# Optimization experiments

Measured on AMD Instinct MI355X. Metric: run time of the kernel, lower is better.

Reference implementation:

```python
import jax, jax.numpy as jnp
import numpy as np

DIM = 768
NUM_HEADS = 12
HEAD_DIM = DIM // NUM_HEADS
SCALE = HEAD_DIM ** -0.5
NEG = -9e15


def setup_inputs() -> dict:
    key = jax.random.key(0)
    ks = jax.random.split(key, 8)
    B, N, M, C = 4, 1024, 2048, DIM
    q = jax.random.normal(ks[0], (B, N, C), dtype=jnp.float32)
    kv = jax.random.normal(ks[1], (B, M, C), dtype=jnp.float32)
    mask = jax.random.randint(ks[2], (B, 1, N, M), 0, 2, dtype=jnp.int32)
    s = 1.0 / np.sqrt(C)
    Wq = jax.random.normal(ks[3], (C, C), dtype=jnp.float32) * s      # nn.Linear(dim, dim), no bias
    Wkv = jax.random.normal(ks[4], (2 * C, C), dtype=jnp.float32) * s  # nn.Linear(dim, 2*dim), no bias
    Wproj = jax.random.normal(ks[5], (C, C), dtype=jnp.float32) * s
    bproj = jax.random.normal(ks[6], (C,), dtype=jnp.float32) * s
    return {"q": q, "kv": kv, "Wq": Wq, "Wkv": Wkv, "Wproj": Wproj, "bproj": bproj, "mask": mask}


def reference(q, kv, Wq, Wkv, Wproj, bproj, mask):
    B, M, C = kv.shape
    _, N, _ = q.shape
    H, d = NUM_HEADS, HEAD_DIM
    # kv projection -> [B, M, 2, H, d] -> k, v: [B, H, M, d]
    kvp = (kv @ Wkv.T).reshape(B, M, 2, H, d)
    k = kvp[:, :, 0].transpose(0, 2, 1, 3)
    v = kvp[:, :, 1].transpose(0, 2, 1, 3)
    # q projection -> [B, H, N, d], pre-scaled
    qp = (q @ Wq.T).reshape(B, N, H, d).transpose(0, 2, 1, 3) * SCALE
    attn = jnp.einsum('bhnd,bhmd->bhnm', qp, k)  # [B, H, N, M]
    attn = jnp.where(mask == 0, NEG, attn)
    attn = jax.nn.softmax(attn, axis=-1)
    # attn_drop / proj_drop have rate 0.0 (eval): identity
    x = jnp.einsum('bhnm,bhmd->bhnd', attn, v)
    x = x.transpose(0, 2, 1, 3).reshape(B, N, C)
    x = x @ Wproj.T + bproj
    return x
```

## Files before the change

### kernel.cpp

```cpp
#include <hip/hip_runtime.h>
#include <hip/hip_bf16.h>


typedef short    s16x8  __attribute__((ext_vector_type(8)));
typedef short    s16x4  __attribute__((ext_vector_type(4)));
typedef float    f32x4  __attribute__((ext_vector_type(4)));
typedef _Float16 f16x8  __attribute__((ext_vector_type(8)));
typedef _Float16 f16x4  __attribute__((ext_vector_type(4)));
typedef _Float16 f16x2  __attribute__((ext_vector_type(2)));

#define NUM_H 12
#define DIM   768
#define NQ    1024
#define MK    2048
#define QK_SCALE_LOG2E 0.18033688f

__device__ __forceinline__ short f2h(float v) {
    _Float16 h = (_Float16)v;
    return __builtin_bit_cast(short, h);
}
__device__ __forceinline__ f32x4 mfma16x32(f16x8 a, f16x8 b, f32x4 c) {
    return __builtin_amdgcn_mfma_f32_16x16x32_f16(a, b, c, 0, 0, 0);
}
__device__ __forceinline__ f16x2 pk2h(float a, float b) {
    return __builtin_bit_cast(f16x2, __builtin_amdgcn_cvt_pkrtz(a, b));
}
__device__ __forceinline__ void gl_lds16(const short* g, short* l) {
    __builtin_amdgcn_global_load_lds(
        (const __attribute__((address_space(1))) unsigned int*)g,
        (__attribute__((address_space(3))) unsigned int*)l, 16, 0, 0);
}

__global__ __launch_bounds__(256) void prep_kernel(
    const float* __restrict__ q, const float* __restrict__ kv,
    const float* __restrict__ Wq, const float* __restrict__ Wkv,
    const float* __restrict__ Wp,
    short* __restrict__ q_h, short* __restrict__ kv_h,
    short* __restrict__ Wq_h, short* __restrict__ Wkv_h,
    short* __restrict__ Wp_h)
{
    int bid = blockIdx.x;
    const float* s; short* d; long base;
    if (bid < 1536)      { s = q;   d = q_h;   base = (long)bid * 2048; }
    else if (bid < 4608) { s = kv;  d = kv_h;  base = (long)(bid - 1536) * 2048; }
    else if (bid < 4896) { s = Wq;  d = Wq_h;  base = (long)(bid - 4608) * 2048; }
    else if (bid < 5472) { s = Wkv; d = Wkv_h; base = (long)(bid - 4896) * 2048; }
    else                 { s = Wp;  d = Wp_h;  base = (long)(bid - 5472) * 2048; }
    long i = base + threadIdx.x * 8;
    float4 a = *(const float4*)(s + i);
    float4 b = *(const float4*)(s + i + 4);
    s16x8 r;
    r[0] = f2h(a.x); r[1] = f2h(a.y); r[2] = f2h(a.z); r[3] = f2h(a.w);
    r[4] = f2h(b.x); r[5] = f2h(b.y); r[6] = f2h(b.z); r[7] = f2h(b.w);
    *(s16x8*)(d + i) = r;
}

__device__ __forceinline__ void gemm_core(
    short* smem,
    const short* __restrict__ A, const short* __restrict__ Bt,
    int mtiles, int mode, const float* __restrict__ bias,
    short* __restrict__ outb, short* __restrict__ outb2,
    float* __restrict__ outf, int bid)
{
    short (*As)[64] = (short(*)[64])smem;
    short (*Bs)[64] = (short(*)[64])(smem + 8192);

    int m0 = (bid % mtiles) << 7;
    int n0 = (bid / mtiles) << 7;
    int t = threadIdx.x;
    int w = t >> 6, lane = t & 63, quad = lane >> 4, l16 = lane & 15;
    int wm = (w & 1) << 6, wn = (w >> 1) << 6;

    f32x4 zero4 = {0.f, 0.f, 0.f, 0.f};
    f32x4 acc[4][4];
    for (int i = 0; i < 4; i++)
        for (int j = 0; j < 4; j++) acc[i][j] = zero4;

    const short* Ag = A + (long)(m0 + (w << 5) + (lane >> 3)) * DIM + ((lane & 7) << 3);
    const short* Bg = Bt + (long)(n0 + (w << 5) + (lane >> 3)) * DIM + ((lane & 7) << 3);
    short* Al = &As[w << 5][0];
    short* Bl = &Bs[w << 5][0];

    for (int kt = 0; kt < DIM; kt += 64) {
        __syncthreads();
        #pragma unroll
        for (int i = 0; i < 4; i++) {
            gl_lds16(Ag + (long)i * 8 * DIM + kt, Al + i * 512);
            gl_lds16(Bg + (long)i * 8 * DIM + kt, Bl + i * 512);
        }
        __syncthreads();
        #pragma unroll
        for (int kh = 0; kh < 2; kh++) {
            f16x8 af[4], bfr[4];
            #pragma unroll
            for (int i = 0; i < 4; i++)
                af[i] = __builtin_bit_cast(f16x8,
                    *(const s16x8*)&As[wm + i * 16 + l16][kh * 32 + quad * 8]);
            #pragma unroll
            for (int j = 0; j < 4; j++)
                bfr[j] = __builtin_bit_cast(f16x8,
                    *(const s16x8*)&Bs[wn + j * 16 + l16][kh * 32 + quad * 8]);
            #pragma unroll
            for (int i = 0; i < 4; i++)
                #pragma unroll
                for (int j = 0; j < 4; j++)
                    acc[i][j] = mfma16x32(af[i], bfr[j], acc[i][j]);
        }
    }

    __syncthreads();

    if (mode == 2) {
        #pragma unroll
        for (int i = 0; i < 4; i++)
            #pragma unroll
            for (int j = 0; j < 4; j++)
                #pragma unroll
                for (int r = 0; r < 4; r++) {
                    int row = m0 + wm + i * 16 + quad * 4 + r;
                    int col = n0 + wn + j * 16 + l16;
                    outf[(long)row * DIM + col] = acc[i][j][r] + bias[col];
                }
        return;
    }

    short (*Cs)[136] = (short(*)[136])smem;
    bool vreg = (mode == 1) && (n0 >= DIM);

    if (!vreg) {
        float sc = (mode == 0) ? QK_SCALE_LOG2E : 1.0f;
        #pragma unroll
        for (int i = 0; i < 4; i++)
            #pragma unroll
            for (int j = 0; j < 4; j++)
                #pragma unroll
                for (int r = 0; r < 4; r++)
                    Cs[wm + i * 16 + quad * 4 + r][wn + j * 16 + l16] =
                        f2h(acc[i][j][r] * sc);
    } else {
        #pragma unroll
        for (int i = 0; i < 4; i++)
            #pragma unroll
            for (int j = 0; j < 4; j++) {
                int c = wn + j * 16 + l16;
                int r0 = wm + i * 16 + quad * 4;
                s16x4 pk;
                pk[0] = f2h(acc[i][j][0]); pk[1] = f2h(acc[i][j][1]);
                pk[2] = f2h(acc[i][j][2]); pk[3] = f2h(acc[i][j][3]);
                *(s16x4*)&Cs[c][r0] = pk;
            }
    }
    __syncthreads();

    if (!vreg) {
        int hb2 = n0 >> 6;
        long rowsN = (mode == 0) ? NQ : MK;
        int b = (int)(m0 / rowsN);
        int rb = (int)(m0 % rowsN);
        short* ob0 = outb + ((long)(b * NUM_H + hb2) * rowsN + rb) * 64;
        short* ob1 = outb + ((long)(b * NUM_H + hb2 + 1) * rowsN + rb) * 64;
        #pragma unroll
        for (int k2 = 0; k2 < 8; k2++) {
            int ch = k2 * 256 + t;
            int half = ch >> 10, off = ch & 1023;
            s16x8 vd = *(const s16x8*)&Cs[off >> 3][(half << 6) + ((off & 7) << 3)];
            *(s16x8*)((half ? ob1 : ob0) + off * 8) = vd;
        }
    } else {
        int hb2 = (n0 - DIM) >> 6;
        int b = m0 >> 11, rb = m0 & 2047;
        #pragma unroll
        for (int k2 = 0; k2 < 8; k2++) {
            int ch = k2 * 256 + t;
            int c = ch >> 4, woff = (ch & 15) << 3;
            s16x8 vd = *(const s16x8*)&Cs[c][woff];
            int half = c >> 6, dd = c & 63;
            *(s16x8*)(outb2 + (((long)(b * NUM_H + hb2 + half) * 64 + dd) * MK + rb) + woff) = vd;
        }
    }
}

__global__ __launch_bounds__(256) void gemm12_kernel(
    const short* __restrict__ qh, const short* __restrict__ Wqh,
    const short* __restrict__ kvh, const short* __restrict__ Wkvh,
    short* __restrict__ qp, short* __restrict__ kk, short* __restrict__ vt,
    const int* __restrict__ mask, unsigned char* __restrict__ mbytes)
{
    __shared__ short smem[18432];
    int bid = blockIdx.x;
    if (bid >= 960) {
        long base = (long)(bid - 960) * 2048 + threadIdx.x * 8;
        int4 m0 = *(const int4*)(mask + base);
        int4 m1 = *(const int4*)(mask + base + 4);
        unsigned v = (unsigned)(m0.x != 0)        | ((unsigned)(m0.y != 0) << 1)
                   | ((unsigned)(m0.z != 0) << 2) | ((unsigned)(m0.w != 0) << 3)
                   | ((unsigned)(m1.x != 0) << 4) | ((unsigned)(m1.y != 0) << 5)
                   | ((unsigned)(m1.z != 0) << 6) | ((unsigned)(m1.w != 0) << 7);
        mbytes[base >> 3] = (unsigned char)v;
        return;
    }
    if (bid < 192)
        gemm_core(smem, qh, Wqh, 32, 0, nullptr, qp, nullptr, nullptr, bid);
    else
        gemm_core(smem, kvh, Wkvh, 64, 1, nullptr, kk, vt, nullptr, bid - 192);
}

__global__ __launch_bounds__(256) void gemm3_kernel(
    const short* __restrict__ xb, const short* __restrict__ Wph,
    const float* __restrict__ bias, float* __restrict__ out)
{
    __shared__ short smem[18432];
    gemm_core(smem, xb, Wph, 32, 2, bias, nullptr, nullptr, out, blockIdx.x);
}

__global__ __launch_bounds__(256) void attn_kernel(
    const short* __restrict__ qp, const short* __restrict__ kk,
    const short* __restrict__ vt, const unsigned* __restrict__ mb,
    short* __restrict__ xb)
{
    __shared__ short qs[64][72];
    __shared__ short ks[64][72];
    __shared__ short vs[64][72];

    int bid = blockIdx.x;
    int bh = bid % 48;
    int nt = bid / 48;
    int h = bh % NUM_H, b = bh / NUM_H;
    int n0 = nt << 6;
    int t = threadIdx.x, w = t >> 6, lane = t & 63, quad = lane >> 4, l16 = lane & 15;

    const short* qbase = qp + ((long)bh * NQ + n0) * 64;
    const short* kbase = kk + (long)bh * MK * 64;
    const short* vbase = vt + (long)bh * 64 * MK;
    const unsigned* mrow = mb + ((long)b * NQ + n0 + (w << 4) + l16) * 64;

    {
        int qr = t >> 2, c0 = (t & 3) << 4;
        *(s16x8*)&qs[qr][c0]     = *(const s16x8*)(qbase + qr * 64 + c0);
        *(s16x8*)&qs[qr][c0 + 8] = *(const s16x8*)(qbase + qr * 64 + c0 + 8);
    }
    __syncthreads();
    f16x8 bq[2];
    #pragma unroll
    for (int kh = 0; kh < 2; kh++)
        bq[kh] = __builtin_bit_cast(f16x8,
            *(const s16x8*)&qs[(w << 4) + l16][kh * 32 + quad * 8]);

    int sr = t >> 2, c0 = (t & 3) << 4;
    int pr = (sr & 32) + ((sr & 4) << 2) + ((sr & 24) >> 1) + (sr & 3);
    const short* kp = kbase + (long)sr * 64 + c0;
    const short* vp = vbase + (long)sr * MK + c0;

    s16x8 k0 = *(const s16x8*)(kp);
    s16x8 k1 = *(const s16x8*)(kp + 8);
    s16x8 v0 = *(const s16x8*)(vp);
    s16x8 v1 = *(const s16x8*)(vp + 8);
    uint2 mwv = *(const uint2*)(mrow);

    f32x4 zero4 = {0.f, 0.f, 0.f, 0.f};
    f32x4 o[4], ol = zero4;
    for (int j = 0; j < 4; j++) o[j] = zero4;
    const f16x8 ones = {(_Float16)1.f, (_Float16)1.f, (_Float16)1.f, (_Float16)1.f,
                        (_Float16)1.f, (_Float16)1.f, (_Float16)1.f, (_Float16)1.f};

    for (int mt = 0; mt < MK; mt += 64) {
        __syncthreads();
        *(s16x8*)&ks[pr][c0]     = k0;
        *(s16x8*)&ks[pr][c0 + 8] = k1;
        *(s16x8*)&vs[sr][c0]     = v0;
        *(s16x8*)&vs[sr][c0 + 8] = v1;
        unsigned cm0 = mwv.x, cm1 = mwv.y;
        __syncthreads();
        if (mt + 64 < MK) {
            k0 = *(const s16x8*)(kp + (long)(mt + 64) * 64);
            k1 = *(const s16x8*)(kp + (long)(mt + 64) * 64 + 8);
            v0 = *(const s16x8*)(vp + mt + 64);
            v1 = *(const s16x8*)(vp + mt + 64 + 8);
            mwv = *(const uint2*)(mrow + ((mt + 64) >> 5));
        }

        f32x4 s[4];
        #pragma unroll
        for (int jj = 0; jj < 4; jj++) s[jj] = zero4;
        #pragma unroll
        for (int kh = 0; kh < 2; kh++)
            #pragma unroll
            for (int jj = 0; jj < 4; jj++) {
                f16x8 ak = __builtin_bit_cast(f16x8,
                    *(const s16x8*)&ks[jj * 16 + l16][kh * 32 + quad * 8]);
                s[jj] = mfma16x32(ak, bq[kh], s[jj]);
            }

        f16x8 pa[2];
        #pragma unroll
        for (int j2 = 0; j2 < 2; j2++) {
            unsigned wsel = j2 ? cm1 : cm0;
            f16x2 pk[4];
            #pragma unroll
            for (int sub = 0; sub < 2; sub++) {
                unsigned bits = wsel >> ((quad << 3) + (sub << 2));
                const f32x4& sv = s[j2 * 2 + sub];
                float p0 = (bits & 1u)        ? __builtin_amdgcn_exp2f(sv[0]) : 0.f;
                float p1 = ((bits >> 1) & 1u) ? __builtin_amdgcn_exp2f(sv[1]) : 0.f;
                float p2 = ((bits >> 2) & 1u) ? __builtin_amdgcn_exp2f(sv[2]) : 0.f;
                float p3 = ((bits >> 3) & 1u) ? __builtin_amdgcn_exp2f(sv[3]) : 0.f;
                pk[sub * 2]     = pk2h(p0, p1);
                pk[sub * 2 + 1] = pk2h(p2, p3);
            }
            f16x4 lo = __builtin_shufflevector(pk[0], pk[1], 0, 1, 2, 3);
            f16x4 hi = __builtin_shufflevector(pk[2], pk[3], 0, 1, 2, 3);
            pa[j2] = __builtin_shufflevector(lo, hi, 0, 1, 2, 3, 4, 5, 6, 7);
        }

        #pragma unroll
        for (int j2 = 0; j2 < 2; j2++) {
            ol = mfma16x32(pa[j2], ones, ol);
            #pragma unroll
            for (int jd = 0; jd < 4; jd++) {
                f16x8 bv = __builtin_bit_cast(f16x8,
                    *(const s16x8*)&vs[jd * 16 + l16][j2 * 32 + quad * 8]);
                o[jd] = mfma16x32(pa[j2], bv, o[jd]);
            }
        }
    }

    float linv[4];
    #pragma unroll
    for (int rr = 0; rr < 4; rr++) linv[rr] = 1.0f / ol[rr];
    short (*ps)[72] = (short(*)[72])&qs[w << 4];
    #pragma unroll
    for (int jd = 0; jd < 4; jd++)
        #pragma unroll
        for (int rr = 0; rr < 4; rr++)
            ps[quad * 4 + rr][jd * 16 + l16] = f2h(o[jd][rr] * linv[rr]);

    #pragma unroll
    for (int k2 = 0; k2 < 2; k2++) {
        int row = (lane >> 3) + k2 * 8;
        int cc = (lane & 7) << 3;
        s16x8 vd = *(const s16x8*)&ps[row][cc];
        *(s16x8*)(xb + ((long)b * NQ + n0 + (w << 4) + row) * DIM + h * 64 + cc) = vd;
    }
}

extern "C" void kernel_launch(void* const* d_in, const int* in_sizes, int n_in,
                              void* d_out, int out_size, void* d_ws, size_t ws_size,
                              hipStream_t stream)
{
    const float* q     = (const float*)d_in[0];
    const float* kv    = (const float*)d_in[1];
    const float* Wq    = (const float*)d_in[2];
    const float* Wkv   = (const float*)d_in[3];
    const float* Wproj = (const float*)d_in[4];
    const float* bproj = (const float*)d_in[5];
    const int*   mask  = (const int*)d_in[6];
    float* out = (float*)d_out;

    char* ws = (char*)d_ws;
    short* q_h   = (short*)ws; ws += (size_t)4096 * 768 * 2;
    short* kv_h  = (short*)ws; ws += (size_t)8192 * 768 * 2;
    short* Wq_h  = (short*)ws; ws += (size_t)768 * 768 * 2;
    short* Wkv_h = (short*)ws; ws += (size_t)1536 * 768 * 2;
    short* Wp_h  = (short*)ws; ws += (size_t)768 * 768 * 2;
    short* qp    = (short*)ws; ws += (size_t)4096 * 768 * 2;
    short* kk    = (short*)ws; ws += (size_t)8192 * 768 * 2;
    short* vt    = (short*)ws; ws += (size_t)8192 * 768 * 2;
    short* xb    = (short*)ws; ws += (size_t)4096 * 768 * 2;
    unsigned char* mbytes = (unsigned char*)ws;

    prep_kernel<<<5760, 256, 0, stream>>>(q, kv, Wq, Wkv, Wproj,
                                          q_h, kv_h, Wq_h, Wkv_h, Wp_h);
    gemm12_kernel<<<5056, 256, 0, stream>>>(q_h, Wq_h, kv_h, Wkv_h,
                                            qp, kk, vt, mask, mbytes);
    attn_kernel<<<768, 256, 0, stream>>>(qp, kk, vt, (const unsigned*)mbytes, xb);
    gemm3_kernel<<<192, 256, 0, stream>>>(xb, Wp_h, bproj, out);
}
```

Before: 222.0 us.

## Fuse fp32-to-fp16 conversion into GEMM tile loads and drop prep kernel

Removes the separate prep kernel that converted inputs and weights to fp16. The GEMMs now load fp32 tiles into registers, convert them in-register and store them to padded LDS. Each next tile is prefetched into registers during compute, replacing the global_load_lds path. This saves a launch and a full fp16 round trip through memory. In exchange, weights are reconverted by every block, register pressure rises, and the direct-to-LDS async loads are lost.

```diff
diff --git a/kernel.cpp b/kernel.cpp
--- a/kernel.cpp
+++ b/kernel.cpp
@@ -25,45 +25,22 @@
 __device__ __forceinline__ f16x2 pk2h(float a, float b) {
     return __builtin_bit_cast(f16x2, __builtin_amdgcn_cvt_pkrtz(a, b));
 }
-__device__ __forceinline__ void gl_lds16(const short* g, short* l) {
-    __builtin_amdgcn_global_load_lds(
-        (const __attribute__((address_space(1))) unsigned int*)g,
-        (__attribute__((address_space(3))) unsigned int*)l, 16, 0, 0);
-}
-
-__global__ __launch_bounds__(256) void prep_kernel(
-    const float* __restrict__ q, const float* __restrict__ kv,
-    const float* __restrict__ Wq, const float* __restrict__ Wkv,
-    const float* __restrict__ Wp,
-    short* __restrict__ q_h, short* __restrict__ kv_h,
-    short* __restrict__ Wq_h, short* __restrict__ Wkv_h,
-    short* __restrict__ Wp_h)
-{
-    int bid = blockIdx.x;
-    const float* s; short* d; long base;
-    if (bid < 1536)      { s = q;   d = q_h;   base = (long)bid * 2048; }
-    else if (bid < 4608) { s = kv;  d = kv_h;  base = (long)(bid - 1536) * 2048; }
-    else if (bid < 4896) { s = Wq;  d = Wq_h;  base = (long)(bid - 4608) * 2048; }
-    else if (bid < 5472) { s = Wkv; d = Wkv_h; base = (long)(bid - 4896) * 2048; }
-    else                 { s = Wp;  d = Wp_h;  base = (long)(bid - 5472) * 2048; }
-    long i = base + threadIdx.x * 8;
-    float4 a = *(const float4*)(s + i);
-    float4 b = *(const float4*)(s + i + 4);
+__device__ __forceinline__ s16x8 cvt8(float4 a, float4 b) {
     s16x8 r;
     r[0] = f2h(a.x); r[1] = f2h(a.y); r[2] = f2h(a.z); r[3] = f2h(a.w);
     r[4] = f2h(b.x); r[5] = f2h(b.y); r[6] = f2h(b.z); r[7] = f2h(b.w);
-    *(s16x8*)(d + i) = r;
-}
-
+    return r;
+}
+
+template<bool A32>
 __device__ __forceinline__ void gemm_core(
-    short* smem,
-    const short* __restrict__ A, const short* __restrict__ Bt,
+    short* smem, const void* Aptr, const float* Btf,
     int mtiles, int mode, const float* __restrict__ bias,
     short* __restrict__ outb, short* __restrict__ outb2,
     float* __restrict__ outf, int bid)
 {
-    short (*As)[64] = (short(*)[64])smem;
-    short (*Bs)[64] = (short(*)[64])(smem + 8192);
+    short (*As)[72] = (short(*)[72])smem;
+    short (*Bs)[72] = (short(*)[72])(smem + 9216);
 
     int m0 = (bid % mtiles) << 7;
     int n0 = (bid / mtiles) << 7;
@@ -76,19 +53,46 @@
     for (int i = 0; i < 4; i++)
         for (int j = 0; j < 4; j++) acc[i][j] = zero4;
 
-    const short* Ag = A + (long)(m0 + (w << 5) + (lane >> 3)) * DIM + ((lane & 7) << 3);
-    const short* Bg = Bt + (long)(n0 + (w << 5) + (lane >> 3)) * DIM + ((lane & 7) << 3);
-    short* Al = &As[w << 5][0];
-    short* Bl = &Bs[w << 5][0];
+    int lr = t >> 1;
+    int lc = (t & 1) << 5;
+    const float* Af = (const float*)Aptr + (long)(m0 + lr) * DIM + lc;
+    const short* Ah = (const short*)Aptr + (long)(m0 + lr) * DIM + lc;
+    const float* Bf = Btf + (long)(n0 + lr) * DIM + lc;
+
+    float4 a32[8]; s16x8 a16[4]; float4 b32[8];
+    if (A32) {
+        #pragma unroll
+        for (int c = 0; c < 8; c++) a32[c] = *(const float4*)(Af + c * 4);
+    } else {
+        #pragma unroll
+        for (int c = 0; c < 4; c++) a16[c] = *(const s16x8*)(Ah + c * 8);
+    }
+    #pragma unroll
+    for (int c = 0; c < 8; c++) b32[c] = *(const float4*)(Bf + c * 4);
 
     for (int kt = 0; kt < DIM; kt += 64) {
         __syncthreads();
         #pragma unroll
-        for (int i = 0; i < 4; i++) {
-            gl_lds16(Ag + (long)i * 8 * DIM + kt, Al + i * 512);
-            gl_lds16(Bg + (long)i * 8 * DIM + kt, Bl + i * 512);
+        for (int c = 0; c < 4; c++) {
+            s16x8 av = A32 ? cvt8(a32[2 * c], a32[2 * c + 1]) : a16[c];
+            *(s16x8*)&As[lr][lc + c * 8] = av;
+            *(s16x8*)&Bs[lr][lc + c * 8] = cvt8(b32[2 * c], b32[2 * c + 1]);
         }
         __syncthreads();
+        if (kt + 64 < DIM) {
+            if (A32) {
+                #pragma unroll
+                for (int c = 0; c < 8; c++)
+                    a32[c] = *(const float4*)(Af + kt + 64 + c * 4);
+            } else {
+                #pragma unroll
+                for (int c = 0; c < 4; c++)
+                    a16[c] = *(const s16x8*)(Ah + kt + 64 + c * 8);
+            }
+            #pragma unroll
+            for (int c = 0; c < 8; c++)
+                b32[c] = *(const float4*)(Bf + kt + 64 + c * 4);
+        }
         #pragma unroll
         for (int kh = 0; kh < 2; kh++) {
             f16x8 af[4], bfr[4];
@@ -181,8 +185,8 @@
 }
 
 __global__ __launch_bounds__(256) void gemm12_kernel(
-    const short* __restrict__ qh, const short* __restrict__ Wqh,
-    const short* __restrict__ kvh, const short* __restrict__ Wkvh,
+    const float* __restrict__ q, const float* __restrict__ Wq,
+    const float* __restrict__ kv, const float* __restrict__ Wkv,
     short* __restrict__ qp, short* __restrict__ kk, short* __restrict__ vt,
     const int* __restrict__ mask, unsigned char* __restrict__ mbytes)
 {
@@ -200,17 +204,17 @@
         return;
     }
     if (bid < 192)
-        gemm_core(smem, qh, Wqh, 32, 0, nullptr, qp, nullptr, nullptr, bid);
+        gemm_core<true>(smem, q, Wq, 32, 0, nullptr, qp, nullptr, nullptr, bid);
     else
-        gemm_core(smem, kvh, Wkvh, 64, 1, nullptr, kk, vt, nullptr, bid - 192);
+        gemm_core<true>(smem, kv, Wkv, 64, 1, nullptr, kk, vt, nullptr, bid - 192);
 }
 
 __global__ __launch_bounds__(256) void gemm3_kernel(
-    const short* __restrict__ xb, const short* __restrict__ Wph,
+    const short* __restrict__ xb, const float* __restrict__ Wp,
     const float* __restrict__ bias, float* __restrict__ out)
 {
     __shared__ short smem[18432];
-    gemm_core(smem, xb, Wph, 32, 2, bias, nullptr, nullptr, out, blockIdx.x);
+    gemm_core<false>(smem, xb, Wp, 32, 2, bias, nullptr, nullptr, out, blockIdx.x);
 }
 
 __global__ __launch_bounds__(256) void attn_kernel(
@@ -357,21 +361,14 @@
     float* out = (float*)d_out;
 
     char* ws = (char*)d_ws;
-    short* q_h   = (short*)ws; ws += (size_t)4096 * 768 * 2;
-    short* kv_h  = (short*)ws; ws += (size_t)8192 * 768 * 2;
-    short* Wq_h  = (short*)ws; ws += (size_t)768 * 768 * 2;
-    short* Wkv_h = (short*)ws; ws += (size_t)1536 * 768 * 2;
-    short* Wp_h  = (short*)ws; ws += (size_t)768 * 768 * 2;
-    short* qp    = (short*)ws; ws += (size_t)4096 * 768 * 2;
-    short* kk    = (short*)ws; ws += (size_t)8192 * 768 * 2;
-    short* vt    = (short*)ws; ws += (size_t)8192 * 768 * 2;
-    short* xb    = (short*)ws; ws += (size_t)4096 * 768 * 2;
+    short* qp = (short*)ws; ws += (size_t)4096 * 768 * 2;
+    short* kk = (short*)ws; ws += (size_t)8192 * 768 * 2;
+    short* vt = (short*)ws; ws += (size_t)8192 * 768 * 2;
+    short* xb = (short*)ws; ws += (size_t)4096 * 768 * 2;
     unsigned char* mbytes = (unsigned char*)ws;
 
-    prep_kernel<<<5760, 256, 0, stream>>>(q, kv, Wq, Wkv, Wproj,
-                                          q_h, kv_h, Wq_h, Wkv_h, Wp_h);
-    gemm12_kernel<<<5056, 256, 0, stream>>>(q_h, Wq_h, kv_h, Wkv_h,
+    gemm12_kernel<<<5056, 256, 0, stream>>>(q, Wq, kv, Wkv,
                                             qp, kk, vt, mask, mbytes);
     attn_kernel<<<768, 256, 0, stream>>>(qp, kk, vt, (const unsigned*)mbytes, xb);
-    gemm3_kernel<<<192, 256, 0, stream>>>(xb, Wp_h, bproj, out);
-}
+    gemm3_kernel<<<192, 256, 0, stream>>>(xb, Wproj, bproj, out);
+}
```

Measured after the change: 265.0 us. 1.19x slower.
